# Kernel tuning notes

Hardware: AMD Instinct MI355X
Metric: run time of the kernel (lower is better)

Reference implementation:

```python
import jax, jax.numpy as jnp
import numpy as np

N = 100000
K = 10  # number of propagation hops


def setup_inputs() -> dict:
    key = jax.random.key(0)
    k1, k2, k3, k4 = jax.random.split(key, 4)
    E, D = 3200000, 128
    feats = jax.random.normal(k1, (N, D), dtype=jnp.float32)
    s = jax.random.normal(k2, (D, 1), dtype=jnp.float32) * 0.1
    src = jax.random.randint(k3, (E,), 0, N, dtype=jnp.int32)
    dst = jax.random.randint(k4, (E,), 0, N, dtype=jnp.int32)
    return {"feats": feats, "s": s, "src": src, "dst": dst}


def reference(feats, s, src, dst):
    # degrees (in-degree = count of dst, out-degree = count of src)
    ones = jnp.ones(src.shape[0], dtype=jnp.float32)
    in_deg = jax.ops.segment_sum(ones, dst, num_segments=N)
    out_deg = jax.ops.segment_sum(ones, src, num_segments=N)
    dst_norm = jnp.clip(in_deg, 1.0, None) ** -0.5  # [N]
    src_norm = jnp.clip(out_deg, 1.0, None) ** -0.5  # [N]
    dst_norm = dst_norm[:, None]
    src_norm = src_norm[:, None]

    results = [feats]
    h = feats
    for _ in range(K):
        h = h * src_norm                                  # [N, D]
        msg = h[src]                                      # gather  [E, D]
        h = jax.ops.segment_sum(msg, dst, num_segments=N)  # scatter [N, D]
        h = h * dst_norm
        results.append(h)

    H = jnp.stack(results, axis=1)                 # [N, K+1, D]
    S = jax.nn.sigmoid(jnp.matmul(H, s))           # [N, K+1, 1]
    S = jnp.transpose(S, (0, 2, 1))                # [N, 1, K+1]
    out = jnp.matmul(S, H).squeeze()               # [N, D]
    return out
```

## Files before the change

### kernel.cpp

```cpp
#include <hip/hip_runtime.h>
#include <hip/hip_fp16.h>

#define NODES 100000
#define DIM 128
#define KSTEPS 10
#define CAP 128

__global__ void build_kernel(const int* __restrict__ src, const int* __restrict__ dst,
                             int* __restrict__ outc, int* __restrict__ cur,
                             int* __restrict__ csr, int E) {
    int i = blockIdx.x * blockDim.x + threadIdx.x;
    int stride = gridDim.x * blockDim.x;
    for (; i < E; i += stride) {
        int s_ = src[i];
        int d_ = dst[i];
        atomicAdd(&outc[s_], 1);
        int c = atomicAdd(&cur[d_], 1);
        if (c < CAP) csr[((size_t)d_ << 7) + c] = s_;
    }
}

__global__ void norm_kernel(const int* __restrict__ outc, const int* __restrict__ inc,
                            float* __restrict__ src_norm, float* __restrict__ isrc,
                            float* __restrict__ dst_norm, int n) {
    int i = blockIdx.x * blockDim.x + threadIdx.x;
    if (i < n) {
        float od = fmaxf((float)outc[i], 1.0f);
        float id = fmaxf((float)inc[i], 1.0f);
        float sn = rsqrtf(od);
        src_norm[i] = sn;
        isrc[i] = sqrtf(od);
        dst_norm[i] = rsqrtf(id);
    }
}

__global__ void combine0_main(const float* __restrict__ feats, const float* __restrict__ s,
                              const float* __restrict__ src_norm,
                              __half* __restrict__ p0, float* __restrict__ sg0, int n) {
    int lane = threadIdx.x & 63;
    int wave = (blockIdx.x * blockDim.x + threadIdx.x) >> 6;
    int nwaves = (gridDim.x * blockDim.x) >> 6;
    float2 sv = *(const float2*)(s + lane * 2);
    for (int node = wave; node < n; node += nwaves) {
        float2 hv = *(const float2*)(feats + (size_t)node * DIM + lane * 2);
        float sn = src_norm[node];
        __half2 ph; ph.x = __float2half(sn * hv.x); ph.y = __float2half(sn * hv.y);
        *(__half2*)(p0 + (size_t)node * DIM + lane * 2) = ph;
        float dot = hv.x * sv.x + hv.y * sv.y;
        #pragma unroll
        for (int off = 32; off > 0; off >>= 1) dot += __shfl_xor(dot, off);
        if (lane == 0) sg0[node] = 1.0f / (1.0f + expf(-dot));
    }
}

__global__ void combine0_fb(const float* __restrict__ feats, const float* __restrict__ s,
                            const float* __restrict__ src_norm,
                            __half* __restrict__ p0, float* __restrict__ out, int n) {
    int lane = threadIdx.x & 63;
    int wave = (blockIdx.x * blockDim.x + threadIdx.x) >> 6;
    int nwaves = (gridDim.x * blockDim.x) >> 6;
    float2 sv = *(const float2*)(s + lane * 2);
    for (int node = wave; node < n; node += nwaves) {
        float2 hv = *(const float2*)(feats + (size_t)node * DIM + lane * 2);
        float sn = src_norm[node];
        __half2 ph; ph.x = __float2half(sn * hv.x); ph.y = __float2half(sn * hv.y);
        *(__half2*)(p0 + (size_t)node * DIM + lane * 2) = ph;
        float dot = hv.x * sv.x + hv.y * sv.y;
        #pragma unroll
        for (int off = 32; off > 0; off >>= 1) dot += __shfl_xor(dot, off);
        float sg = 1.0f / (1.0f + expf(-dot));
        float2 ov; ov.x = sg * hv.x; ov.y = sg * hv.y;
        *(float2*)(out + (size_t)node * DIM + lane * 2) = ov;
    }
}

__global__ void gather_main(const __half* __restrict__ pprev,
                            const float* __restrict__ src_norm, const float* __restrict__ dst_norm,
                            const int* __restrict__ cnt, const int* __restrict__ csr,
                            const float* __restrict__ s,
                            __half* __restrict__ pnext, float* __restrict__ sgk, int n) {
    int lane = threadIdx.x & 63;
    int wave = (blockIdx.x * blockDim.x + threadIdx.x) >> 6;
    int nwaves = (gridDim.x * blockDim.x) >> 6;
    float2 sv = *(const float2*)(s + lane * 2);
    for (int node = wave; node < n; node += nwaves) {
        int c = cnt[node]; if (c > CAP) c = CAP;
        const int* row = csr + ((size_t)node << 7);
        float accx = 0.0f, accy = 0.0f;
        int p = 0;
        for (; p + 7 < c; p += 8) {
            int s0 = row[p], s1 = row[p+1], s2 = row[p+2], s3 = row[p+3];
            int s4 = row[p+4], s5 = row[p+5], s6 = row[p+6], s7 = row[p+7];
            float2 f0 = __half22float2(*(const __half2*)(pprev + (size_t)s0 * DIM + lane * 2));
            float2 f1 = __half22float2(*(const __half2*)(pprev + (size_t)s1 * DIM + lane * 2));
            float2 f2 = __half22float2(*(const __half2*)(pprev + (size_t)s2 * DIM + lane * 2));
            float2 f3 = __half22float2(*(const __half2*)(pprev + (size_t)s3 * DIM + lane * 2));
            float2 f4 = __half22float2(*(const __half2*)(pprev + (size_t)s4 * DIM + lane * 2));
            float2 f5 = __half22float2(*(const __half2*)(pprev + (size_t)s5 * DIM + lane * 2));
            float2 f6 = __half22float2(*(const __half2*)(pprev + (size_t)s6 * DIM + lane * 2));
            float2 f7 = __half22float2(*(const __half2*)(pprev + (size_t)s7 * DIM + lane * 2));
            accx += f0.x + f1.x + f2.x + f3.x + f4.x + f5.x + f6.x + f7.x;
            accy += f0.y + f1.y + f2.y + f3.y + f4.y + f5.y + f6.y + f7.y;
        }
        for (; p < c; ++p) {
            int si = row[p];
            float2 fv = __half22float2(*(const __half2*)(pprev + (size_t)si * DIM + lane * 2));
            accx += fv.x; accy += fv.y;
        }
        float dn = dst_norm[node];
        float hx = dn * accx, hy = dn * accy;
        float dot = hx * sv.x + hy * sv.y;
        #pragma unroll
        for (int off = 32; off > 0; off >>= 1) dot += __shfl_xor(dot, off);
        if (lane == 0) sgk[node] = 1.0f / (1.0f + expf(-dot));
        float sn = src_norm[node];
        __half2 pw; pw.x = __float2half(sn * hx); pw.y = __float2half(sn * hy);
        *(__half2*)(pnext + (size_t)node * DIM + lane * 2) = pw;
    }
}

__global__ void gather_fb(const __half* __restrict__ pprev,
                          const float* __restrict__ src_norm, const float* __restrict__ dst_norm,
                          const int* __restrict__ cnt, const int* __restrict__ csr,
                          const float* __restrict__ s,
                          __half* __restrict__ pnext, float* __restrict__ out, int n) {
    int lane = threadIdx.x & 63;
    int wave = (blockIdx.x * blockDim.x + threadIdx.x) >> 6;
    int nwaves = (gridDim.x * blockDim.x) >> 6;
    float2 sv = *(const float2*)(s + lane * 2);
    for (int node = wave; node < n; node += nwaves) {
        int c = cnt[node]; if (c > CAP) c = CAP;
        const int* row = csr + ((size_t)node << 7);
        float accx = 0.0f, accy = 0.0f;
        int p = 0;
        for (; p + 7 < c; p += 8) {
            int s0 = row[p], s1 = row[p+1], s2 = row[p+2], s3 = row[p+3];
            int s4 = row[p+4], s5 = row[p+5], s6 = row[p+6], s7 = row[p+7];
            float2 f0 = __half22float2(*(const __half2*)(pprev + (size_t)s0 * DIM + lane * 2));
            float2 f1 = __half22float2(*(const __half2*)(pprev + (size_t)s1 * DIM + lane * 2));
            float2 f2 = __half22float2(*(const __half2*)(pprev + (size_t)s2 * DIM + lane * 2));
            float2 f3 = __half22float2(*(const __half2*)(pprev + (size_t)s3 * DIM + lane * 2));
            float2 f4 = __half22float2(*(const __half2*)(pprev + (size_t)s4 * DIM + lane * 2));
            float2 f5 = __half22float2(*(const __half2*)(pprev + (size_t)s5 * DIM + lane * 2));
            float2 f6 = __half22float2(*(const __half2*)(pprev + (size_t)s6 * DIM + lane * 2));
            float2 f7 = __half22float2(*(const __half2*)(pprev + (size_t)s7 * DIM + lane * 2));
            accx += f0.x + f1.x + f2.x + f3.x + f4.x + f5.x + f6.x + f7.x;
            accy += f0.y + f1.y + f2.y + f3.y + f4.y + f5.y + f6.y + f7.y;
        }
        for (; p < c; ++p) {
            int si = row[p];
            float2 fv = __half22float2(*(const __half2*)(pprev + (size_t)si * DIM + lane * 2));
            accx += fv.x; accy += fv.y;
        }
        float dn = dst_norm[node];
        float hx = dn * accx, hy = dn * accy;
        float dot = hx * sv.x + hy * sv.y;
        #pragma unroll
        for (int off = 32; off > 0; off >>= 1) dot += __shfl_xor(dot, off);
        float sg = 1.0f / (1.0f + expf(-dot));
        float2 ov = *(float2*)(out + (size_t)node * DIM + lane * 2);
        ov.x += sg * hx; ov.y += sg * hy;
        *(float2*)(out + (size_t)node * DIM + lane * 2) = ov;
        float sn = src_norm[node];
        __half2 pw; pw.x = __float2half(sn * hx); pw.y = __float2half(sn * hy);
        *(__half2*)(pnext + (size_t)node * DIM + lane * 2) = pw;
    }
}

__global__ void final_combine(const __half* __restrict__ pbase, const float* __restrict__ sg,
                              const float* __restrict__ isrc, float* __restrict__ out, int n) {
    int lane = threadIdx.x & 63;
    int wave = (blockIdx.x * blockDim.x + threadIdx.x) >> 6;
    int nwaves = (gridDim.x * blockDim.x) >> 6;
    for (int node = wave; node < n; node += nwaves) {
        float iv = isrc[node];
        float ax = 0.0f, ay = 0.0f;
        #pragma unroll
        for (int k = 0; k <= KSTEPS; ++k) {
            float g = sg[(size_t)k * n + node] * iv;
            float2 fv = __half22float2(
                *(const __half2*)(pbase + ((size_t)k * n + node) * DIM + lane * 2));
            ax += g * fv.x; ay += g * fv.y;
        }
        *(float2*)(out + (size_t)node * DIM + lane * 2) = make_float2(ax, ay);
    }
}

extern "C" void kernel_launch(void* const* d_in, const int* in_sizes, int n_in,
                              void* d_out, int out_size, void* d_ws, size_t ws_size,
                              hipStream_t stream) {
    const float* feats = (const float*)d_in[0];
    const float* s     = (const float*)d_in[1];
    const int*   src   = (const int*)d_in[2];
    const int*   dst   = (const int*)d_in[3];
    float* out = (float*)d_out;
    const int E = in_sizes[2];

    int*   outc     = (int*)d_ws;
    int*   cur      = outc + NODES;
    float* src_norm = (float*)(cur + NODES);
    float* isrc     = src_norm + NODES;
    float* dst_norm = isrc + NODES;
    float* sg       = dst_norm + NODES;
    int*   csr      = (int*)(sg + (size_t)(KSTEPS + 1) * NODES);
    __half* pbase   = (__half*)(csr + (size_t)NODES * CAP);

    const size_t head_bytes = (size_t)(2 * NODES) * 4 + (size_t)(3 + KSTEPS + 1) * NODES * 4
                            + (size_t)NODES * CAP * 4;
    const size_t pbuf = (size_t)NODES * DIM * sizeof(__half);
    const bool main_path = ws_size >= head_bytes + (size_t)(KSTEPS + 1) * pbuf;

    hipMemsetAsync(outc, 0, 2 * NODES * sizeof(int), stream);
    build_kernel<<<2048, 256, 0, stream>>>(src, dst, outc, cur, csr, E);
    norm_kernel<<<(NODES + 255) / 256, 256, 0, stream>>>(outc, cur, src_norm, isrc, dst_norm, NODES);

    const int ngrid = (NODES * 64 + 255) / 256;
    if (main_path) {
        combine0_main<<<ngrid, 256, 0, stream>>>(feats, s, src_norm, pbase, sg, NODES);
        for (int k = 1; k <= KSTEPS; ++k) {
            const __half* pprev = pbase + (size_t)(k - 1) * NODES * DIM;
            __half* pnext = pbase + (size_t)k * NODES * DIM;
            gather_main<<<ngrid, 256, 0, stream>>>(pprev, src_norm, dst_norm, cur, csr, s,
                                                   pnext, sg + (size_t)k * NODES, NODES);
        }
        final_combine<<<ngrid, 256, 0, stream>>>(pbase, sg, isrc, out, NODES);
    } else {
        __half* pA = pbase;
        __half* pB = pbase + (size_t)NODES * DIM;
        combine0_fb<<<ngrid, 256, 0, stream>>>(feats, s, src_norm, pA, out, NODES);
        const __half* pcur = pA;
        for (int k = 1; k <= KSTEPS; ++k) {
            __half* pnext = (k & 1) ? pB : pA;
            gather_fb<<<ngrid, 256, 0, stream>>>(pcur, src_norm, dst_norm, cur, csr, s,
                                                 pnext, out, NODES);
            pcur = pnext;
        }
    }
}
```

Baseline: 1.676 ms.

## Split feature planes into 8 slices for cache-resident gather per hop

Stores the propagated half-precision features as eight separate 16-dim slice planes (32 bytes per node each). Each gather block handles one slice, so a hop's random-access working set is a 3.2MB plane that can stay in cache instead of the full 25.6MB table. Each wave processes eight edges in parallel, and the per-hop sigmoid scores move into the final combine, which now reads all slice planes. The trade-off is that the CSR index rows are re-read once per slice, eight times per hop.

```diff
diff --git a/kernel.cpp b/kernel.cpp
--- a/kernel.cpp
+++ b/kernel.cpp
@@ -5,6 +5,8 @@
 #define DIM 128
 #define KSTEPS 10
 #define CAP 128
+#define NSLICE 8
+#define SLICE_H2 8
 
 __global__ void build_kernel(const int* __restrict__ src, const int* __restrict__ dst,
                              int* __restrict__ outc, int* __restrict__ cur,
@@ -21,35 +23,90 @@
 }
 
 __global__ void norm_kernel(const int* __restrict__ outc, const int* __restrict__ inc,
-                            float* __restrict__ src_norm, float* __restrict__ isrc,
-                            float* __restrict__ dst_norm, int n) {
+                            float* __restrict__ src_norm, float* __restrict__ dsn,
+                            float* __restrict__ isrc, float* __restrict__ dstn, int n) {
     int i = blockIdx.x * blockDim.x + threadIdx.x;
     if (i < n) {
         float od = fmaxf((float)outc[i], 1.0f);
         float id = fmaxf((float)inc[i], 1.0f);
         float sn = rsqrtf(od);
+        float dn = rsqrtf(id);
         src_norm[i] = sn;
         isrc[i] = sqrtf(od);
-        dst_norm[i] = rsqrtf(id);
-    }
-}
-
-__global__ void combine0_main(const float* __restrict__ feats, const float* __restrict__ s,
-                              const float* __restrict__ src_norm,
-                              __half* __restrict__ p0, float* __restrict__ sg0, int n) {
-    int lane = threadIdx.x & 63;
-    int wave = (blockIdx.x * blockDim.x + threadIdx.x) >> 6;
-    int nwaves = (gridDim.x * blockDim.x) >> 6;
-    float2 sv = *(const float2*)(s + lane * 2);
+        dsn[i] = sn * dn;
+        dstn[i] = dn;
+    }
+}
+
+__global__ void combine0_main(const float* __restrict__ feats, const float* __restrict__ src_norm,
+                              __half2* __restrict__ pbase, int n) {
+    int lane = threadIdx.x & 63;
+    int wave = (blockIdx.x * blockDim.x + threadIdx.x) >> 6;
+    int nwaves = (gridDim.x * blockDim.x) >> 6;
+    int sl = lane >> 3, dp = lane & 7;
     for (int node = wave; node < n; node += nwaves) {
         float2 hv = *(const float2*)(feats + (size_t)node * DIM + lane * 2);
         float sn = src_norm[node];
         __half2 ph; ph.x = __float2half(sn * hv.x); ph.y = __float2half(sn * hv.y);
-        *(__half2*)(p0 + (size_t)node * DIM + lane * 2) = ph;
-        float dot = hv.x * sv.x + hv.y * sv.y;
+        pbase[((size_t)sl * n + node) * SLICE_H2 + dp] = ph;
+    }
+}
+
+__global__ void gather_slice(const __half2* __restrict__ pprev, const float* __restrict__ dsn,
+                             const int* __restrict__ cnt, const int* __restrict__ csr,
+                             __half2* __restrict__ pnext, int n) {
+    int slice = blockIdx.x & 7;
+    int blk = blockIdx.x >> 3;
+    int lane = threadIdx.x & 63;
+    int waveid = threadIdx.x >> 6;
+    int nwaves = (gridDim.x >> 3) << 2;
+    int wave = (blk << 2) + waveid;
+    int dp = lane & 7;
+    int eg = lane >> 3;
+    const __half2* plane_prev = pprev + (size_t)slice * n * SLICE_H2;
+    __half2* plane_next = pnext + (size_t)slice * n * SLICE_H2;
+    for (int node = wave; node < n; node += nwaves) {
+        int c = cnt[node]; if (c > CAP) c = CAP;
+        const int* row = csr + ((size_t)node << 7);
+        float ax = 0.0f, ay = 0.0f;
+        for (int p = eg; p < c; p += 8) {
+            int si = row[p];
+            float2 f = __half22float2(plane_prev[(size_t)si * SLICE_H2 + dp]);
+            ax += f.x; ay += f.y;
+        }
+        ax += __shfl_xor(ax, 8);  ay += __shfl_xor(ay, 8);
+        ax += __shfl_xor(ax, 16); ay += __shfl_xor(ay, 16);
+        ax += __shfl_xor(ax, 32); ay += __shfl_xor(ay, 32);
+        if (eg == 0) {
+            float sc = dsn[node];
+            __half2 pw; pw.x = __float2half(sc * ax); pw.y = __float2half(sc * ay);
+            plane_next[(size_t)node * SLICE_H2 + dp] = pw;
+        }
+    }
+}
+
+__global__ void final_combine(const __half2* __restrict__ pbase, const float* __restrict__ isrc,
+                              const float* __restrict__ s, float* __restrict__ out, int n) {
+    int lane = threadIdx.x & 63;
+    int wave = (blockIdx.x * blockDim.x + threadIdx.x) >> 6;
+    int nwaves = (gridDim.x * blockDim.x) >> 6;
+    int sl = lane >> 3, dp = lane & 7;
+    float2 sv = *(const float2*)(s + lane * 2);
+    for (int node = wave; node < n; node += nwaves) {
+        float iv = isrc[node];
+        float ax = 0.0f, ay = 0.0f;
         #pragma unroll
-        for (int off = 32; off > 0; off >>= 1) dot += __shfl_xor(dot, off);
-        if (lane == 0) sg0[node] = 1.0f / (1.0f + expf(-dot));
+        for (int k = 0; k <= KSTEPS; ++k) {
+            float2 f = __half22float2(
+                pbase[((size_t)(k * NSLICE + sl) * n + node) * SLICE_H2 + dp]);
+            float hx = iv * f.x, hy = iv * f.y;
+            float dot = hx * sv.x + hy * sv.y;
+            #pragma unroll
+            for (int off = 32; off > 0; off >>= 1) dot += __shfl_xor(dot, off);
+            float sg = 1.0f / (1.0f + expf(-dot));
+            ax += sg * hx; ay += sg * hy;
+        }
+        *(float2*)(out + (size_t)node * DIM + lane * 2) = make_float2(ax, ay);
     }
 }
 
@@ -74,11 +131,11 @@
     }
 }
 
-__global__ void gather_main(const __half* __restrict__ pprev,
-                            const float* __restrict__ src_norm, const float* __restrict__ dst_norm,
-                            const int* __restrict__ cnt, const int* __restrict__ csr,
-                            const float* __restrict__ s,
-                            __half* __restrict__ pnext, float* __restrict__ sgk, int n) {
+__global__ void gather_fb(const __half* __restrict__ pprev,
+                          const float* __restrict__ dsn, const float* __restrict__ dstn,
+                          const int* __restrict__ cnt, const int* __restrict__ csr,
+                          const float* __restrict__ s,
+                          __half* __restrict__ pnext, float* __restrict__ out, int n) {
     int lane = threadIdx.x & 63;
     int wave = (blockIdx.x * blockDim.x + threadIdx.x) >> 6;
     int nwaves = (gridDim.x * blockDim.x) >> 6;
@@ -88,72 +145,21 @@
         const int* row = csr + ((size_t)node << 7);
         float accx = 0.0f, accy = 0.0f;
         int p = 0;
-        for (; p + 7 < c; p += 8) {
+        for (; p + 3 < c; p += 4) {
             int s0 = row[p], s1 = row[p+1], s2 = row[p+2], s3 = row[p+3];
-            int s4 = row[p+4], s5 = row[p+5], s6 = row[p+6], s7 = row[p+7];
             float2 f0 = __half22float2(*(const __half2*)(pprev + (size_t)s0 * DIM + lane * 2));
             float2 f1 = __half22float2(*(const __half2*)(pprev + (size_t)s1 * DIM + lane * 2));
             float2 f2 = __half22float2(*(const __half2*)(pprev + (size_t)s2 * DIM + lane * 2));
             float2 f3 = __half22float2(*(const __half2*)(pprev + (size_t)s3 * DIM + lane * 2));
-            float2 f4 = __half22float2(*(const __half2*)(pprev + (size_t)s4 * DIM + lane * 2));
-            float2 f5 = __half22float2(*(const __half2*)(pprev + (size_t)s5 * DIM + lane * 2));
-            float2 f6 = __half22float2(*(const __half2*)(pprev + (size_t)s6 * DIM + lane * 2));
-            float2 f7 = __half22float2(*(const __half2*)(pprev + (size_t)s7 * DIM + lane * 2));
-            accx += f0.x + f1.x + f2.x + f3.x + f4.x + f5.x + f6.x + f7.x;
-            accy += f0.y + f1.y + f2.y + f3.y + f4.y + f5.y + f6.y + f7.y;
+            accx += f0.x + f1.x + f2.x + f3.x;
+            accy += f0.y + f1.y + f2.y + f3.y;
         }
         for (; p < c; ++p) {
             int si = row[p];
             float2 fv = __half22float2(*(const __half2*)(pprev + (size_t)si * DIM + lane * 2));
             accx += fv.x; accy += fv.y;
         }
-        float dn = dst_norm[node];
-        float hx = dn * accx, hy = dn * accy;
-        float dot = hx * sv.x + hy * sv.y;
-        #pragma unroll
-        for (int off = 32; off > 0; off >>= 1) dot += __shfl_xor(dot, off);
-        if (lane == 0) sgk[node] = 1.0f / (1.0f + expf(-dot));
-        float sn = src_norm[node];
-        __half2 pw; pw.x = __float2half(sn * hx); pw.y = __float2half(sn * hy);
-        *(__half2*)(pnext + (size_t)node * DIM + lane * 2) = pw;
-    }
-}
-
-__global__ void gather_fb(const __half* __restrict__ pprev,
-                          const float* __restrict__ src_norm, const float* __restrict__ dst_norm,
-                          const int* __restrict__ cnt, const int* __restrict__ csr,
-                          const float* __restrict__ s,
-                          __half* __restrict__ pnext, float* __restrict__ out, int n) {
-    int lane = threadIdx.x & 63;
-    int wave = (blockIdx.x * blockDim.x + threadIdx.x) >> 6;
-    int nwaves = (gridDim.x * blockDim.x) >> 6;
-    float2 sv = *(const float2*)(s + lane * 2);
-    for (int node = wave; node < n; node += nwaves) {
-        int c = cnt[node]; if (c > CAP) c = CAP;
-        const int* row = csr + ((size_t)node << 7);
-        float accx = 0.0f, accy = 0.0f;
-        int p = 0;
-        for (; p + 7 < c; p += 8) {
-            int s0 = row[p], s1 = row[p+1], s2 = row[p+2], s3 = row[p+3];
-            int s4 = row[p+4], s5 = row[p+5], s6 = row[p+6], s7 = row[p+7];
-            float2 f0 = __half22float2(*(const __half2*)(pprev + (size_t)s0 * DIM + lane * 2));
-            float2 f1 = __half22float2(*(const __half2*)(pprev + (size_t)s1 * DIM + lane * 2));
-            float2 f2 = __half22float2(*(const __half2*)(pprev + (size_t)s2 * DIM + lane * 2));
-            float2 f3 = __half22float2(*(const __half2*)(pprev + (size_t)s3 * DIM + lane * 2));
-            float2 f4 = __half22float2(*(const __half2*)(pprev + (size_t)s4 * DIM + lane * 2));
-            float2 f5 = __half22float2(*(const __half2*)(pprev + (size_t)s5 * DIM + lane * 2));
-            float2 f6 = __half22float2(*(const __half2*)(pprev + (size_t)s6 * DIM + lane * 2));
-            float2 f7 = __half22float2(*(const __half2*)(pprev + (size_t)s7 * DIM + lane * 2));
-            accx += f0.x + f1.x + f2.x + f3.x + f4.x + f5.x + f6.x + f7.x;
-            accy += f0.y + f1.y + f2.y + f3.y + f4.y + f5.y + f6.y + f7.y;
-        }
-        for (; p < c; ++p) {
-            int si = row[p];
-            float2 fv = __half22float2(*(const __half2*)(pprev + (size_t)si * DIM + lane * 2));
-            accx += fv.x; accy += fv.y;
-        }
-        float dn = dst_norm[node];
-        float hx = dn * accx, hy = dn * accy;
+        float hx = dstn[node] * accx, hy = dstn[node] * accy;
         float dot = hx * sv.x + hy * sv.y;
         #pragma unroll
         for (int off = 32; off > 0; off >>= 1) dot += __shfl_xor(dot, off);
@@ -161,28 +167,9 @@
         float2 ov = *(float2*)(out + (size_t)node * DIM + lane * 2);
         ov.x += sg * hx; ov.y += sg * hy;
         *(float2*)(out + (size_t)node * DIM + lane * 2) = ov;
-        float sn = src_norm[node];
-        __half2 pw; pw.x = __float2half(sn * hx); pw.y = __float2half(sn * hy);
+        float sc = dsn[node];
+        __half2 pw; pw.x = __float2half(sc * accx); pw.y = __float2half(sc * accy);
         *(__half2*)(pnext + (size_t)node * DIM + lane * 2) = pw;
-    }
-}
-
-__global__ void final_combine(const __half* __restrict__ pbase, const float* __restrict__ sg,
-                              const float* __restrict__ isrc, float* __restrict__ out, int n) {
-    int lane = threadIdx.x & 63;
-    int wave = (blockIdx.x * blockDim.x + threadIdx.x) >> 6;
-    int nwaves = (gridDim.x * blockDim.x) >> 6;
-    for (int node = wave; node < n; node += nwaves) {
-        float iv = isrc[node];
-        float ax = 0.0f, ay = 0.0f;
-        #pragma unroll
-        for (int k = 0; k <= KSTEPS; ++k) {
-            float g = sg[(size_t)k * n + node] * iv;
-            float2 fv = __half22float2(
-                *(const __half2*)(pbase + ((size_t)k * n + node) * DIM + lane * 2));
-            ax += g * fv.x; ay += g * fv.y;
-        }
-        *(float2*)(out + (size_t)node * DIM + lane * 2) = make_float2(ax, ay);
     }
 }
 
@@ -199,39 +186,38 @@
     int*   outc     = (int*)d_ws;
     int*   cur      = outc + NODES;
     float* src_norm = (float*)(cur + NODES);
-    float* isrc     = src_norm + NODES;
-    float* dst_norm = isrc + NODES;
-    float* sg       = dst_norm + NODES;
-    int*   csr      = (int*)(sg + (size_t)(KSTEPS + 1) * NODES);
-    __half* pbase   = (__half*)(csr + (size_t)NODES * CAP);
-
-    const size_t head_bytes = (size_t)(2 * NODES) * 4 + (size_t)(3 + KSTEPS + 1) * NODES * 4
-                            + (size_t)NODES * CAP * 4;
+    float* dsn      = src_norm + NODES;
+    float* isrc     = dsn + NODES;
+    float* dstn     = isrc + NODES;
+    int*   csr      = (int*)(dstn + NODES);
+    __half2* pbase  = (__half2*)(csr + (size_t)NODES * CAP);
+
+    const size_t head_bytes = (size_t)(6 * NODES) * 4 + (size_t)NODES * CAP * 4;
     const size_t pbuf = (size_t)NODES * DIM * sizeof(__half);
     const bool main_path = ws_size >= head_bytes + (size_t)(KSTEPS + 1) * pbuf;
 
     hipMemsetAsync(outc, 0, 2 * NODES * sizeof(int), stream);
     build_kernel<<<2048, 256, 0, stream>>>(src, dst, outc, cur, csr, E);
-    norm_kernel<<<(NODES + 255) / 256, 256, 0, stream>>>(outc, cur, src_norm, isrc, dst_norm, NODES);
+    norm_kernel<<<(NODES + 255) / 256, 256, 0, stream>>>(outc, cur, src_norm, dsn, isrc, dstn, NODES);
 
     const int ngrid = (NODES * 64 + 255) / 256;
     if (main_path) {
-        combine0_main<<<ngrid, 256, 0, stream>>>(feats, s, src_norm, pbase, sg, NODES);
+        combine0_main<<<ngrid, 256, 0, stream>>>(feats, src_norm, pbase, NODES);
+        const size_t kstride = (size_t)NSLICE * NODES * SLICE_H2;
         for (int k = 1; k <= KSTEPS; ++k) {
-            const __half* pprev = pbase + (size_t)(k - 1) * NODES * DIM;
-            __half* pnext = pbase + (size_t)k * NODES * DIM;
-            gather_main<<<ngrid, 256, 0, stream>>>(pprev, src_norm, dst_norm, cur, csr, s,
-                                                   pnext, sg + (size_t)k * NODES, NODES);
-        }
-        final_combine<<<ngrid, 256, 0, stream>>>(pbase, sg, isrc, out, NODES);
+            gather_slice<<<8192, 256, 0, stream>>>(
+                pbase + (size_t)(k - 1) * kstride, dsn, cur, csr,
+                pbase + (size_t)k * kstride, NODES);
+        }
+        final_combine<<<ngrid, 256, 0, stream>>>(pbase, isrc, s, out, NODES);
     } else {
-        __half* pA = pbase;
-        __half* pB = pbase + (size_t)NODES * DIM;
+        __half* pA = (__half*)pbase;
+        __half* pB = pA + (size_t)NODES * DIM;
         combine0_fb<<<ngrid, 256, 0, stream>>>(feats, s, src_norm, pA, out, NODES);
         const __half* pcur = pA;
         for (int k = 1; k <= KSTEPS; ++k) {
             __half* pnext = (k & 1) ? pB : pA;
-            gather_fb<<<ngrid, 256, 0, stream>>>(pcur, src_norm, dst_norm, cur, csr, s,
+            gather_fb<<<ngrid, 256, 0, stream>>>(pcur, dsn, dstn, cur, csr, s,
                                                  pnext, out, NODES);
             pcur = pnext;
         }
```

After: 1.746 ms. 4.1% more time.
